# Kernel optimization log

Hardware: AMD Instinct MI355X
Metric: run time of the kernel (lower is better)

## Reference

```python
import jax, jax.numpy as jnp
import numpy as np

B, S, T = 32, 64, 48
E = 128          # embed size
H = 256          # encoder hidden (per direction)
HD = 512         # decoder hidden = 2*H
V = 32001        # vocab_size + 1


def setup_inputs() -> dict:
    key = jax.random.key(0)
    ks = jax.random.split(key, 20)
    p = lambda k, shp: jax.random.normal(k, shp, dtype=jnp.float32) * 0.05
    inp = {}
    inp["input_sequence"] = jax.random.randint(ks[0], (B, S), 0, V)
    lengths = jax.random.randint(ks[1], (B,), 1, S + 1).at[0].set(S)
    inp["input_seq_lengths"] = lengths
    inp["output_sequence"] = jax.random.randint(ks[2], (B, T), 0, V)
    # encoder params
    inp["emb_src"] = p(ks[3], (V, E))
    inp["Wih_f"] = p(ks[4], (4 * H, E)); inp["Whh_f"] = p(ks[5], (4 * H, H)); inp["b_f"] = p(ks[6], (4 * H,))
    inp["Wih_b"] = p(ks[7], (4 * H, E)); inp["Whh_b"] = p(ks[8], (4 * H, H)); inp["b_b"] = p(ks[9], (4 * H,))
    # decoder params
    inp["emb_tgt"] = p(ks[10], (V, E))
    inp["Wih_d"] = p(ks[11], (4 * HD, E)); inp["Whh_d"] = p(ks[12], (4 * HD, HD)); inp["b_d"] = p(ks[13], (4 * HD,))
    inp["W1"] = p(ks[14], (HD, HD)); inp["W2"] = p(ks[15], (HD, HD)); inp["v"] = p(ks[16], (HD,))
    inp["Wo"] = p(ks[17], (V, HD)); inp["bo"] = p(ks[18], (V,))
    return inp


def _cell(x, h, c, Wih, Whh, b):
    # PyTorch LSTM gate order: i, f, g, o. b = b_ih + b_hh.
    g = x @ Wih.T + h @ Whh.T + b
    i, f, gg, o = jnp.split(g, 4, axis=-1)
    c = jax.nn.sigmoid(f) * c + jax.nn.sigmoid(i) * jnp.tanh(gg)
    h = jax.nn.sigmoid(o) * jnp.tanh(c)
    return h, c


def reference(input_sequence, input_seq_lengths, output_sequence,
              emb_src, Wih_f, Whh_f, b_f, Wih_b, Whh_b, b_b,
              emb_tgt, Wih_d, Whh_d, b_d, W1, W2, v, Wo, bo):
    x = emb_src[input_sequence]                       # [B,S,E]
    valid = jnp.arange(S)[None, :] < input_seq_lengths[:, None]  # [B,S]
    xs = jnp.swapaxes(x, 0, 1)                        # [S,B,E]
    vs = valid.T                                      # [S,B]
    z = jnp.zeros((B, H), jnp.float32)

    def fstep(carry, inp):
        h, c = carry
        xt, vt = inp
        h, c = _cell(xt, h, c, Wih_f, Whh_f, b_f)
        return (h, c), jnp.where(vt[:, None], h, 0.0)

    _, of = jax.lax.scan(fstep, (z, z), (xs, vs))

    def bstep(carry, inp):
        # backward direction of a packed LSTM: state starts at each sequence's
        # last valid token (state held at zero while t >= length)
        h, c = carry
        xt, vt = inp
        hn, cn = _cell(xt, h, c, Wih_b, Whh_b, b_b)
        m = vt[:, None]
        h = jnp.where(m, hn, h)
        c = jnp.where(m, cn, c)
        return (h, c), jnp.where(m, h, 0.0)

    _, ob = jax.lax.scan(bstep, (z, z), (xs[::-1], vs[::-1]))
    ob = ob[::-1]
    enc = jnp.swapaxes(jnp.concatenate([of, ob], axis=-1), 0, 1)  # [B,S,512], zeros at pads

    key_proj = enc @ W1.T                             # precompute W1(key): [B,S,512]

    tgt_emb = emb_tgt[output_sequence]                # [B,T,E]
    dec_in = jnp.concatenate([jnp.zeros((B, 1, E), jnp.float32), tgt_emb[:, :-1]], axis=1)
    dec_xs = jnp.swapaxes(dec_in, 0, 1)               # [T,B,E]

    def dstep(carry, xt):
        h, c = carry
        h, c = _cell(xt, h, c, Wih_d, Whh_d, b_d)
        qp = h @ W2.T                                 # [B,512]
        energy = jnp.tanh(key_proj + qp[:, None, :]) @ v   # [B,S]
        energy = jnp.where(valid, energy, -1e10)
        w = jax.nn.softmax(energy, axis=1)
        ctx = jnp.einsum('bs,bsd->bd', w, enc)        # [B,512]
        logits = (h + ctx) @ Wo.T + bo                # [B,V]
        return (h, c), logits

    z2 = jnp.zeros((B, HD), jnp.float32)
    _, logits = jax.lax.scan(dstep, (z2, z2), dec_xs)
    outputs = jnp.swapaxes(logits, 0, 1)              # [B,T,V]

    # CrossEntropyLoss(ignore_index=0), mean over non-ignored targets
    logp = jax.nn.log_softmax(outputs, axis=-1)
    nll = -jnp.take_along_axis(logp, output_sequence[:, :, None], axis=-1)[..., 0]
    m = (output_sequence != 0).astype(jnp.float32)
    loss = jnp.sum(nll * m) / jnp.maximum(jnp.sum(m), 1.0)
    return outputs, loss
```

## Files before the change

### kernel.cpp

```cpp
#include <hip/hip_runtime.h>


typedef unsigned short ushort_t;
typedef unsigned int   uint_t;
typedef __attribute__((ext_vector_type(8))) short bf16x8;
typedef __attribute__((ext_vector_type(4))) float f32x4;

#define DEV static __device__ __forceinline__

#define NB 32
#define NS 64
#define NT 48
#define NE 128
#define NH 256
#define ND 512
#define NV 32001

#define OFF_GF   0ull
#define OFF_GB   8388608ull
#define OFF_GD   16777216ull
#define OFF_KP   29360128ull
#define OFF_CWO  0ull
#define OFF_QP   33554432ull
#define OFF_ENC  36700160ull
#define OFF_HBF  38797312ull
#define OFF_ACTX 40370176ull
#define OFF_XEE  41943040ull
#define OFF_XED  42467328ull
#define OFF_CWF  42860544ull
#define OFF_CWB  43122688ull
#define OFF_CWD  43384832ull
#define OFF_CW1  43909120ull
#define OFF_CW2  44433408ull
#define OFF_HBE  44957696ull
#define OFF_HBD  45023232ull
#define OFF_MISC 45088768ull

DEV float b2f(ushort_t u) { return __uint_as_float(((uint_t)u) << 16); }
DEV ushort_t f2b(float f) {
  uint_t x = __float_as_uint(f);
  return (ushort_t)((x + 0x7fffu + ((x >> 16) & 1u)) >> 16);
}
DEV float fsig(float x) { return 1.f / (1.f + __expf(-x)); }
DEV float ftanh(float x) { float e = __expf(2.f * x); return 1.f - 2.f / (e + 1.f); }

DEV f32x4 mfma16(bf16x8 a, bf16x8 b, f32x4 c) {
  return __builtin_amdgcn_mfma_f32_16x16x32_bf16(a, b, c, 0, 0, 0);
}
DEV void async16(void* lds, const void* g) {
  __builtin_amdgcn_global_load_lds(
      (const __attribute__((address_space(1))) uint_t*)g,
      (__attribute__((address_space(3))) uint_t*)lds, 16, 0, 0);
}
DEV bf16x8 ldw8(const float* p) {
  f32x4 a = *(const f32x4*)p;
  f32x4 b = *(const f32x4*)(p + 4);
  bf16x8 r;
  r[0] = (short)f2b(a[0]); r[1] = (short)f2b(a[1]);
  r[2] = (short)f2b(a[2]); r[3] = (short)f2b(a[3]);
  r[4] = (short)f2b(b[0]); r[5] = (short)f2b(b[1]);
  r[6] = (short)f2b(b[2]); r[7] = (short)f2b(b[3]);
  return r;
}

__global__ void init_ws(uint_t* misc) {
  for (int i = threadIdx.x; i < 1024; i += 256) misc[i] = 0u;
}

__global__ __launch_bounds__(256) void cvt_bf16(const float* __restrict__ src,
                                                ushort_t* __restrict__ dst,
                                                int n4) {
  int i = blockIdx.x * 256 + threadIdx.x;
  if (i < n4) {
    f32x4 x = *(const f32x4*)(src + (size_t)i * 4);
    uint_t lo = ((uint_t)f2b(x[1]) << 16) | (uint_t)f2b(x[0]);
    uint_t hi = ((uint_t)f2b(x[3]) << 16) | (uint_t)f2b(x[2]);
    uint2 v; v.x = lo; v.y = hi;
    *(uint2*)(dst + (size_t)i * 4) = v;
  }
}

__global__ __launch_bounds__(128) void gather_enc(const float* __restrict__ emb,
                                                  const int* __restrict__ seq,
                                                  ushort_t* __restrict__ xe) {
  int m = blockIdx.x;
  int s = m >> 5, b = m & 31;
  int tok = seq[b * NS + s];
  xe[(size_t)m * NE + threadIdx.x] = f2b(emb[(size_t)tok * NE + threadIdx.x]);
}
__global__ __launch_bounds__(128) void gather_dec(const float* __restrict__ emb,
                                                  const int* __restrict__ seq,
                                                  ushort_t* __restrict__ xe) {
  int m = blockIdx.x;
  int t = m >> 5, b = m & 31;
  float v = 0.f;
  if (t > 0) v = emb[(size_t)seq[b * NT + t - 1] * NE + threadIdx.x];
  xe[(size_t)m * NE + threadIdx.x] = f2b(v);
}

template <int CMODE, int BIAS>
__global__ __launch_bounds__(256, 2) void gemm_nt(
    const ushort_t* __restrict__ Abase, const ushort_t* __restrict__ Bmat,
    const float* __restrict__ bias, float* __restrict__ Cf,
    int N, int K, int Nvalid) {
  const int tid = threadIdx.x;
  const int wv = tid >> 6, l = tid & 63, c15 = l & 15, q = l >> 4;
  const int mw = wv >> 1, nw = wv & 1;
  const int n0 = blockIdx.x * 128, m0 = blockIdx.y * 128;
  __shared__ __align__(16) ushort_t lds[32 * 512];

  f32x4 acc[4][4];
  const f32x4 zz = {0.f, 0.f, 0.f, 0.f};
#pragma unroll
  for (int i = 0; i < 4; ++i)
#pragma unroll
    for (int j = 0; j < 4; ++j) acc[i][j] = zz;

  for (int k0 = 0; k0 < K; k0 += 64) {
    __syncthreads();
#pragma unroll
    for (int i = 0; i < 4; ++i) {
      const int slot = wv * 4 + i;
      const int kt = slot >> 3, mt = slot & 7;
      const int m = m0 + mt * 16 + c15;
      async16(&lds[slot * 512], Abase + (size_t)m * K + k0 + kt * 32 + q * 8);
      int n = n0 + mt * 16 + c15;
      if (n >= Nvalid) n = Nvalid - 1;
      async16(&lds[(16 + slot) * 512], Bmat + (size_t)n * K + k0 + kt * 32 + q * 8);
    }
    __syncthreads();
#pragma unroll
    for (int kt = 0; kt < 2; ++kt) {
      bf16x8 af[4], bfr[4];
#pragma unroll
      for (int i = 0; i < 4; ++i)
        af[i] = *(const bf16x8*)&lds[(kt * 8 + mw * 4 + i) * 512 + l * 8];
#pragma unroll
      for (int i = 0; i < 4; ++i)
        bfr[i] = *(const bf16x8*)&lds[(16 + kt * 8 + nw * 4 + i) * 512 + l * 8];
#pragma unroll
      for (int mi = 0; mi < 4; ++mi)
#pragma unroll
        for (int ni = 0; ni < 4; ++ni)
          acc[mi][ni] = mfma16(af[mi], bfr[ni], acc[mi][ni]);
    }
  }
#pragma unroll
  for (int mi = 0; mi < 4; ++mi)
#pragma unroll
    for (int ni = 0; ni < 4; ++ni) {
      const int n = n0 + (nw * 4 + ni) * 16 + c15;
      float bv = 0.f;
      if (BIAS) { if (CMODE != 2 || n < Nvalid) bv = bias[n]; }
#pragma unroll
      for (int r = 0; r < 4; ++r) {
        const int m = m0 + (mw * 4 + mi) * 16 + q * 4 + r;
        const float val = acc[mi][ni][r] + bv;
        if (CMODE == 0) Cf[(size_t)m * N + n] = val;
        else if (CMODE == 1) Cf[((size_t)(m >> 5) * N + n) * 32 + (m & 31)] = val;
        else if (n < Nvalid) Cf[(size_t)m * (size_t)NV + n] = val;
      }
    }
}

__global__ __launch_bounds__(512, 2) void enc_scan(
    const float* __restrict__ WhhF, const float* __restrict__ WhhB,
    const float* __restrict__ gF, const float* __restrict__ gB,
    const int* __restrict__ lens, ushort_t* __restrict__ enc_bf,
    ushort_t* __restrict__ hbuf, int* __restrict__ flags) {
  const int tid = threadIdx.x;
  const int d = blockIdx.x >> 1, p = blockIdx.x & 1;
  const int w = tid >> 6, l = tid & 63, c = l & 15, q = l >> 4;
  const float* Whh = d ? WhhB : WhhF;
  const float* gpre = d ? gB : gF;
  ushort_t* hb_base = hbuf + (size_t)d * 2 * 8192;
  int* flag = flags + d;
  const int u = p * 128 + w * 16 + c;

  bf16x8 wf[4][8];
#pragma unroll
  for (int g = 0; g < 4; ++g)
#pragma unroll
    for (int kt = 0; kt < 8; ++kt)
      wf[g][kt] = ldw8(Whh + (size_t)(g * 256 + u) * 256 + kt * 32 + q * 8);

  __shared__ __align__(16) ushort_t hsh[8192];
  for (int i = tid; i < 8192; i += 512) hsh[i] = 0;
  float cst[8], hst[8];
#pragma unroll
  for (int i = 0; i < 8; ++i) { cst[i] = 0.f; hst[i] = 0.f; }
  int lensr[8];
#pragma unroll
  for (int mt = 0; mt < 2; ++mt)
#pragma unroll
    for (int r = 0; r < 4; ++r) lensr[mt * 4 + r] = lens[mt * 16 + q * 4 + r];
  const int kt_u = u >> 5, j_u = u & 7, hi16 = ((u >> 3) & 3) << 4;
  __syncthreads();

  int tgt = 0;
#pragma unroll 1
  for (int s = 0; s < 64; ++s) {
    const int so = d ? (63 - s) : s;
    f32x4 acc[4][2];
#pragma unroll
    for (int g = 0; g < 4; ++g) {
      const float* gp = gpre + ((size_t)so * 1024 + (g * 256 + u)) * 32 + q * 4;
      acc[g][0] = *(const f32x4*)gp;
      acc[g][1] = *(const f32x4*)(gp + 16);
    }
#pragma unroll
    for (int kt = 0; kt < 8; ++kt) {
      bf16x8 a0 = *(const bf16x8*)&hsh[kt * 512 + l * 8];
      bf16x8 a1 = *(const bf16x8*)&hsh[(8 + kt) * 512 + l * 8];
#pragma unroll
      for (int g = 0; g < 4; ++g) {
        acc[g][0] = mfma16(a0, wf[g][kt], acc[g][0]);
        acc[g][1] = mfma16(a1, wf[g][kt], acc[g][1]);
      }
    }
    ushort_t* hbw = hb_base + (s & 1) * 8192;
#pragma unroll
    for (int mt = 0; mt < 2; ++mt)
#pragma unroll
      for (int r = 0; r < 4; ++r) {
        const int k8 = mt * 4 + r;
        const int bi = mt * 16 + q * 4 + r;
        float gi = acc[0][mt][r], gf = acc[1][mt][r];
        float gg = acc[2][mt][r], go = acc[3][mt][r];
        float ctn = fsig(gf) * cst[k8] + fsig(gi) * ftanh(gg);
        float hn = fsig(go) * ftanh(ctn);
        bool valid = so < lensr[k8];
        bool upd = (d == 0) || valid;
        cst[k8] = upd ? ctn : cst[k8];
        hst[k8] = upd ? hn : hst[k8];
        enc_bf[((size_t)bi * 64 + so) * 512 + d * 256 + u] = f2b(valid ? hn : 0.f);
        hbw[((mt * 8 + kt_u) * 64 + ((bi & 15) | hi16)) * 8 + j_u] = f2b(hst[k8]);
      }
    __syncthreads();
    if (tid == 0)
      __hip_atomic_fetch_add(flag, 1, __ATOMIC_RELEASE, __HIP_MEMORY_SCOPE_AGENT);
    tgt += 2;
    if (tid == 0) {
      while (__hip_atomic_load(flag, __ATOMIC_ACQUIRE, __HIP_MEMORY_SCOPE_AGENT) < tgt)
        __builtin_amdgcn_s_sleep(1);
    }
    __syncthreads();
    (void)__hip_atomic_load(flag, __ATOMIC_ACQUIRE, __HIP_MEMORY_SCOPE_AGENT);
    for (int i = tid; i < 1024; i += 512)
      ((uint4*)hsh)[i] = ((const uint4*)hbw)[i];
    __syncthreads();
  }
}

__global__ __launch_bounds__(512, 2) void dec_scan(
    const float* __restrict__ Whh, const float* __restrict__ gpre,
    ushort_t* __restrict__ h_bf, ushort_t* __restrict__ hbuf,
    int* __restrict__ flag) {
  const int tid = threadIdx.x;
  const int bb = blockIdx.x;
  const int w = tid >> 6, l = tid & 63, c = l & 15, q = l >> 4;
  const int uu = bb * 64 + w * 8 + (c & 7);
  const int row0 = ((c >> 3)) * 512 + uu;
  const int row1 = (2 + (c >> 3)) * 512 + uu;

  bf16x8 wf0[16], wf1[16];
#pragma unroll
  for (int kt = 0; kt < 16; ++kt) {
    wf0[kt] = ldw8(Whh + (size_t)row0 * 512 + kt * 32 + q * 8);
    wf1[kt] = ldw8(Whh + (size_t)row1 * 512 + kt * 32 + q * 8);
  }
  __shared__ __align__(16) ushort_t hsh[16384];
  for (int i = tid; i < 16384; i += 512) hsh[i] = 0;
  float cst[8];
#pragma unroll
  for (int i = 0; i < 8; ++i) cst[i] = 0.f;
  const int kt_u = uu >> 5, j_u = uu & 7, hi16 = ((uu >> 3) & 3) << 4;
  __syncthreads();

  int tgt = 0;
#pragma unroll 1
  for (int t = 0; t < 48; ++t) {
    f32x4 acc[2][2];
    {
      const float* gp0 = gpre + ((size_t)t * 2048 + row0) * 32 + q * 4;
      const float* gp1 = gpre + ((size_t)t * 2048 + row1) * 32 + q * 4;
      acc[0][0] = *(const f32x4*)gp0; acc[0][1] = *(const f32x4*)(gp0 + 16);
      acc[1][0] = *(const f32x4*)gp1; acc[1][1] = *(const f32x4*)(gp1 + 16);
    }
#pragma unroll
    for (int kt = 0; kt < 16; ++kt) {
      bf16x8 a0 = *(const bf16x8*)&hsh[kt * 512 + l * 8];
      bf16x8 a1 = *(const bf16x8*)&hsh[(16 + kt) * 512 + l * 8];
      acc[0][0] = mfma16(a0, wf0[kt], acc[0][0]);
      acc[0][1] = mfma16(a1, wf0[kt], acc[0][1]);
      acc[1][0] = mfma16(a0, wf1[kt], acc[1][0]);
      acc[1][1] = mfma16(a1, wf1[kt], acc[1][1]);
    }
    ushort_t* hbw = hbuf + (t & 1) * 16384;
#pragma unroll
    for (int mt = 0; mt < 2; ++mt)
#pragma unroll
      for (int r = 0; r < 4; ++r) {
        const int k8 = mt * 4 + r;
        const int bi = mt * 16 + q * 4 + r;
        float x0 = acc[0][mt][r];
        float x1 = acc[1][mt][r];
        float Av = fsig(x0) * ftanh(x1);
        float Ar = __shfl_xor(Av, 8, 64);
        if (c >= 8) {
          float ctn = fsig(x0) * cst[k8] + Ar;
          float hn = fsig(x1) * ftanh(ctn);
          cst[k8] = ctn;
          ushort_t hb16 = f2b(hn);
          h_bf[((size_t)t * 32 + bi) * 512 + uu] = hb16;
          hbw[((mt * 16 + kt_u) * 64 + ((bi & 15) | hi16)) * 8 + j_u] = hb16;
        }
      }
    __syncthreads();
    if (tid == 0)
      __hip_atomic_fetch_add(flag, 1, __ATOMIC_RELEASE, __HIP_MEMORY_SCOPE_AGENT);
    tgt += 8;
    if (tid == 0) {
      while (__hip_atomic_load(flag, __ATOMIC_ACQUIRE, __HIP_MEMORY_SCOPE_AGENT) < tgt)
        __builtin_amdgcn_s_sleep(1);
    }
    __syncthreads();
    (void)__hip_atomic_load(flag, __ATOMIC_ACQUIRE, __HIP_MEMORY_SCOPE_AGENT);
    for (int i = tid; i < 2048; i += 512)
      ((uint4*)hsh)[i] = ((const uint4*)hbw)[i];
    __syncthreads();
  }
}

__global__ __launch_bounds__(256) void attn_k(
    const float* __restrict__ qp, const float* __restrict__ kp,
    const ushort_t* __restrict__ enc_bf, const ushort_t* __restrict__ h_bf,
    const float* __restrict__ vvec, const int* __restrict__ lens,
    ushort_t* __restrict__ actx) {
  const int bid = blockIdx.x;
  const int b = bid / NT, t = bid % NT;
  const int tid = threadIdx.x;
  __shared__ float qps[512], vs[512], es[64];
  {
    const float* qrow = qp + ((size_t)t * 32 + b) * 512;
    float2 x = *(const float2*)&qrow[tid * 2];
    qps[tid * 2] = x.x; qps[tid * 2 + 1] = x.y;
    float2 vv = *(const float2*)&vvec[tid * 2];
    vs[tid * 2] = vv.x; vs[tid * 2 + 1] = vv.y;
  }
  __syncthreads();
  const int s = tid >> 2, i = tid & 3;
  const int len = lens[b];
  {
    const float* kr = kp + ((size_t)b * 64 + s) * 512 + i * 128;
    float e = 0.f;
#pragma unroll 8
    for (int k = 0; k < 128; k += 4) {
      f32x4 x = *(const f32x4*)&kr[k];
      const int ko = i * 128 + k;
      e += ftanh(x[0] + qps[ko]) * vs[ko];
      e += ftanh(x[1] + qps[ko + 1]) * vs[ko + 1];
      e += ftanh(x[2] + qps[ko + 2]) * vs[ko + 2];
      e += ftanh(x[3] + qps[ko + 3]) * vs[ko + 3];
    }
    e += __shfl_xor(e, 1, 64);
    e += __shfl_xor(e, 2, 64);
    if (i == 0) es[s] = (s < len) ? e : -1e10f;
  }
  __syncthreads();
  if (tid < 64) {
    float x = es[tid], m = x;
#pragma unroll
    for (int o = 1; o < 64; o <<= 1) m = fmaxf(m, __shfl_xor(m, o, 64));
    float pe = __expf(x - m), sum = pe;
#pragma unroll
    for (int o = 1; o < 64; o <<= 1) sum += __shfl_xor(sum, o, 64);
    es[tid] = pe / sum;
  }
  __syncthreads();
  const int d0 = tid * 2;
  float a0 = 0.f, a1 = 0.f;
  const ushort_t* erow = enc_bf + (size_t)b * 64 * 512 + d0;
#pragma unroll 4
  for (int ss = 0; ss < 64; ++ss) {
    uint_t uv = *(const uint_t*)(erow + (size_t)ss * 512);
    float wgt = es[ss];
    a0 += wgt * b2f((ushort_t)(uv & 0xffff));
    a1 += wgt * b2f((ushort_t)(uv >> 16));
  }
  uint_t hu = *(const uint_t*)(h_bf + ((size_t)t * 32 + b) * 512 + d0);
  float o0 = a0 + b2f((ushort_t)(hu & 0xffff));
  float o1 = a1 + b2f((ushort_t)(hu >> 16));
  uint_t packed = ((uint_t)f2b(o1) << 16) | (uint_t)f2b(o0);
  *(uint_t*)(actx + ((size_t)b * NT + t) * 512 + d0) = packed;
}

__global__ __launch_bounds__(256) void loss_k(const float* __restrict__ outp,
                                              const int* __restrict__ oseq,
                                              float* __restrict__ acc) {
  const int m = blockIdx.x;
  const int b = m / NT, t = m % NT;
  const int tid = threadIdx.x;
  const float* row = outp + (size_t)m * NV;
  __shared__ float redA[4], redB[4];
  float mx = -1e30f;
  for (int v = tid; v < NV; v += 256) mx = fmaxf(mx, row[v]);
#pragma unroll
  for (int o = 32; o; o >>= 1) mx = fmaxf(mx, __shfl_xor(mx, o, 64));
  if ((tid & 63) == 0) redA[tid >> 6] = mx;
  __syncthreads();
  mx = fmaxf(fmaxf(redA[0], redA[1]), fmaxf(redA[2], redA[3]));
  float sm = 0.f;
  for (int v = tid; v < NV; v += 256) sm += __expf(row[v] - mx);
#pragma unroll
  for (int o = 32; o; o >>= 1) sm += __shfl_xor(sm, o, 64);
  if ((tid & 63) == 0) redB[tid >> 6] = sm;
  __syncthreads();
  if (tid == 0) {
    float tot = redB[0] + redB[1] + redB[2] + redB[3];
    float lse = __logf(tot) + mx;
    int tok = oseq[b * NT + t];
    float nll = lse - row[tok];
    if (tok != 0) { atomicAdd(&acc[0], nll); atomicAdd(&acc[1], 1.f); }
  }
}

__global__ void finalize_loss(const float* __restrict__ acc,
                              float* __restrict__ outp) {
  if (threadIdx.x == 0)
    outp[(size_t)NB * NT * NV] = acc[0] / fmaxf(acc[1], 1.f);
}

extern "C" void kernel_launch(void* const* d_in, const int* in_sizes, int n_in,
                              void* d_out, int out_size, void* d_ws,
                              size_t ws_size, hipStream_t stream) {
  (void)in_sizes; (void)n_in; (void)out_size; (void)ws_size;
  const int* in_seq  = (const int*)d_in[0];
  const int* lens    = (const int*)d_in[1];
  const int* out_seq = (const int*)d_in[2];
  const float* emb_src = (const float*)d_in[3];
  const float* Wih_f = (const float*)d_in[4];
  const float* Whh_f = (const float*)d_in[5];
  const float* b_f   = (const float*)d_in[6];
  const float* Wih_b = (const float*)d_in[7];
  const float* Whh_b = (const float*)d_in[8];
  const float* b_b   = (const float*)d_in[9];
  const float* emb_tgt = (const float*)d_in[10];
  const float* Wih_d = (const float*)d_in[11];
  const float* Whh_d = (const float*)d_in[12];
  const float* b_d   = (const float*)d_in[13];
  const float* W1 = (const float*)d_in[14];
  const float* W2 = (const float*)d_in[15];
  const float* vv = (const float*)d_in[16];
  const float* Wo = (const float*)d_in[17];
  const float* bo = (const float*)d_in[18];

  char* ws = (char*)d_ws;
  float* g_fT    = (float*)(ws + OFF_GF);
  float* g_bT    = (float*)(ws + OFF_GB);
  float* g_dT    = (float*)(ws + OFF_GD);
  float* keyp    = (float*)(ws + OFF_KP);
  float* qp      = (float*)(ws + OFF_QP);
  ushort_t* encb = (ushort_t*)(ws + OFF_ENC);
  ushort_t* hbf  = (ushort_t*)(ws + OFF_HBF);
  ushort_t* actx = (ushort_t*)(ws + OFF_ACTX);
  ushort_t* xee  = (ushort_t*)(ws + OFF_XEE);
  ushort_t* xed  = (ushort_t*)(ws + OFF_XED);
  ushort_t* c_wf = (ushort_t*)(ws + OFF_CWF);
  ushort_t* c_wb = (ushort_t*)(ws + OFF_CWB);
  ushort_t* c_wd = (ushort_t*)(ws + OFF_CWD);
  ushort_t* c_w1 = (ushort_t*)(ws + OFF_CW1);
  ushort_t* c_w2 = (ushort_t*)(ws + OFF_CW2);
  ushort_t* c_wo = (ushort_t*)(ws + OFF_CWO);
  ushort_t* hbe  = (ushort_t*)(ws + OFF_HBE);
  ushort_t* hbd  = (ushort_t*)(ws + OFF_HBD);
  int* flags     = (int*)(ws + OFF_MISC);
  float* accp    = (float*)(ws + OFF_MISC + 32);
  float* outp    = (float*)d_out;

  init_ws<<<1, 256, 0, stream>>>((uint_t*)(ws + OFF_MISC));
  gather_enc<<<NB * NS, 128, 0, stream>>>(emb_src, in_seq, xee);
  gather_dec<<<NB * NT, 128, 0, stream>>>(emb_tgt, out_seq, xed);
  cvt_bf16<<<128, 256, 0, stream>>>(Wih_f, c_wf, 32768);
  cvt_bf16<<<128, 256, 0, stream>>>(Wih_b, c_wb, 32768);
  cvt_bf16<<<256, 256, 0, stream>>>(Wih_d, c_wd, 65536);
  cvt_bf16<<<256, 256, 0, stream>>>(W1, c_w1, 65536);
  cvt_bf16<<<256, 256, 0, stream>>>(W2, c_w2, 65536);
  gemm_nt<1, 1><<<dim3(8, 16), 256, 0, stream>>>(
      xee, c_wf, b_f, g_fT, 1024, 128, 1024);
  gemm_nt<1, 1><<<dim3(8, 16), 256, 0, stream>>>(
      xee, c_wb, b_b, g_bT, 1024, 128, 1024);
  gemm_nt<1, 1><<<dim3(16, 12), 256, 0, stream>>>(
      xed, c_wd, b_d, g_dT, 2048, 128, 2048);
  enc_scan<<<4, 512, 0, stream>>>(Whh_f, Whh_b, g_fT, g_bT, lens, encb, hbe, flags);
  gemm_nt<0, 0><<<dim3(4, 16), 256, 0, stream>>>(
      encb, c_w1, nullptr, keyp, 512, 512, 512);
  dec_scan<<<8, 512, 0, stream>>>(Whh_d, g_dT, hbf, hbd, flags + 2);
  gemm_nt<0, 0><<<dim3(4, 12), 256, 0, stream>>>(
      hbf, c_w2, nullptr, qp, 512, 512, 512);
  attn_k<<<NB * NT, 256, 0, stream>>>(qp, keyp, encb, hbf, vv, lens, actx);
  cvt_bf16<<<16001, 256, 0, stream>>>(Wo, c_wo, 4096128);
  gemm_nt<2, 1><<<dim3(251, 12), 256, 0, stream>>>(
      actx, c_wo, bo, outp, NV, 512, NV);
  loss_k<<<NB * NT, 256, 0, stream>>>(outp, out_seq, accp);
  finalize_loss<<<1, 64, 0, stream>>>(accp, outp);
}
```

Measured before the change: 1.465 ms.

## Single-block encoder scan, double-buffered LDS, prefetched gates, online-softmax loss

The encoder scan now runs one 1024-thread block per direction, so the hidden state stays in double-buffered LDS and the global flag-based inter-block barrier is gone. The decoder scan prefetches the next step's gate preactivations and double-buffers its LDS. It now publishes only its own hidden slice, using relaxed agent-scope 8-byte atomics and a vmcnt wait in place of acquire/release ordering. The loss kernel merges the max and sum-exp passes into one online-softmax pass that reads the logits once. In exchange, the relaxed-ordering handshake is riskier to get right, and 1024-thread blocks with large register-resident weights may limit occupancy or spill.

After: 2.250 ms. 53.6% more time.

```diff
diff --git a/kernel.cpp b/kernel.cpp
--- a/kernel.cpp
+++ b/kernel.cpp
@@ -3,6 +3,7 @@
 
 typedef unsigned short ushort_t;
 typedef unsigned int   uint_t;
+typedef unsigned long long ull_t;
 typedef __attribute__((ext_vector_type(8))) short bf16x8;
 typedef __attribute__((ext_vector_type(4))) float f32x4;
 
@@ -63,6 +64,13 @@
   return r;
 }
 
+DEV void st8_cc(void* p, ull_t v) {
+  __hip_atomic_store((ull_t*)p, v, __ATOMIC_RELAXED, __HIP_MEMORY_SCOPE_AGENT);
+}
+DEV ull_t ld8_cc(const void* p) {
+  return __hip_atomic_load((ull_t*)p, __ATOMIC_RELAXED, __HIP_MEMORY_SCOPE_AGENT);
+}
+
 __global__ void init_ws(uint_t* misc) {
   for (int i = threadIdx.x; i < 1024; i += 256) misc[i] = 0u;
 }
@@ -163,19 +171,16 @@
     }
 }
 
-__global__ __launch_bounds__(512, 2) void enc_scan(
+__global__ __launch_bounds__(1024, 1) void enc_scan(
     const float* __restrict__ WhhF, const float* __restrict__ WhhB,
     const float* __restrict__ gF, const float* __restrict__ gB,
-    const int* __restrict__ lens, ushort_t* __restrict__ enc_bf,
-    ushort_t* __restrict__ hbuf, int* __restrict__ flags) {
+    const int* __restrict__ lens, ushort_t* __restrict__ enc_bf) {
   const int tid = threadIdx.x;
-  const int d = blockIdx.x >> 1, p = blockIdx.x & 1;
+  const int d = blockIdx.x;
   const int w = tid >> 6, l = tid & 63, c = l & 15, q = l >> 4;
   const float* Whh = d ? WhhB : WhhF;
   const float* gpre = d ? gB : gF;
-  ushort_t* hb_base = hbuf + (size_t)d * 2 * 8192;
-  int* flag = flags + d;
-  const int u = p * 128 + w * 16 + c;
+  const int u = w * 16 + c;
 
   bf16x8 wf[4][8];
 #pragma unroll
@@ -184,8 +189,8 @@
     for (int kt = 0; kt < 8; ++kt)
       wf[g][kt] = ldw8(Whh + (size_t)(g * 256 + u) * 256 + kt * 32 + q * 8);
 
-  __shared__ __align__(16) ushort_t hsh[8192];
-  for (int i = tid; i < 8192; i += 512) hsh[i] = 0;
+  __shared__ __align__(16) ushort_t hsh[2][8192];
+  for (int i = tid; i < 8192; i += 1024) hsh[0][i] = 0;
   float cst[8], hst[8];
 #pragma unroll
   for (int i = 0; i < 8; ++i) { cst[i] = 0.f; hst[i] = 0.f; }
@@ -195,30 +200,45 @@
 #pragma unroll
     for (int r = 0; r < 4; ++r) lensr[mt * 4 + r] = lens[mt * 16 + q * 4 + r];
   const int kt_u = u >> 5, j_u = u & 7, hi16 = ((u >> 3) & 3) << 4;
+
+  f32x4 gv[4][2];
+  {
+    const int so0 = d ? 63 : 0;
+#pragma unroll
+    for (int g = 0; g < 4; ++g) {
+      const float* gp = gpre + ((size_t)so0 * 1024 + (g * 256 + u)) * 32 + q * 4;
+      gv[g][0] = *(const f32x4*)gp;
+      gv[g][1] = *(const f32x4*)(gp + 16);
+    }
+  }
   __syncthreads();
 
-  int tgt = 0;
 #pragma unroll 1
   for (int s = 0; s < 64; ++s) {
     const int so = d ? (63 - s) : s;
+    const int rb = s & 1;
     f32x4 acc[4][2];
 #pragma unroll
-    for (int g = 0; g < 4; ++g) {
-      const float* gp = gpre + ((size_t)so * 1024 + (g * 256 + u)) * 32 + q * 4;
-      acc[g][0] = *(const f32x4*)gp;
-      acc[g][1] = *(const f32x4*)(gp + 16);
+    for (int g = 0; g < 4; ++g) { acc[g][0] = gv[g][0]; acc[g][1] = gv[g][1]; }
+    if (s < 63) {
+      const int son = d ? (62 - s) : (s + 1);
+#pragma unroll
+      for (int g = 0; g < 4; ++g) {
+        const float* gp = gpre + ((size_t)son * 1024 + (g * 256 + u)) * 32 + q * 4;
+        gv[g][0] = *(const f32x4*)gp;
+        gv[g][1] = *(const f32x4*)(gp + 16);
+      }
     }
 #pragma unroll
     for (int kt = 0; kt < 8; ++kt) {
-      bf16x8 a0 = *(const bf16x8*)&hsh[kt * 512 + l * 8];
-      bf16x8 a1 = *(const bf16x8*)&hsh[(8 + kt) * 512 + l * 8];
+      bf16x8 a0 = *(const bf16x8*)&hsh[rb][kt * 512 + l * 8];
+      bf16x8 a1 = *(const bf16x8*)&hsh[rb][(8 + kt) * 512 + l * 8];
 #pragma unroll
       for (int g = 0; g < 4; ++g) {
         acc[g][0] = mfma16(a0, wf[g][kt], acc[g][0]);
         acc[g][1] = mfma16(a1, wf[g][kt], acc[g][1]);
       }
     }
-    ushort_t* hbw = hb_base + (s & 1) * 8192;
 #pragma unroll
     for (int mt = 0; mt < 2; ++mt)
 #pragma unroll
@@ -234,20 +254,9 @@
         cst[k8] = upd ? ctn : cst[k8];
         hst[k8] = upd ? hn : hst[k8];
         enc_bf[((size_t)bi * 64 + so) * 512 + d * 256 + u] = f2b(valid ? hn : 0.f);
-        hbw[((mt * 8 + kt_u) * 64 + ((bi & 15) | hi16)) * 8 + j_u] = f2b(hst[k8]);
+        hsh[rb ^ 1][((mt * 8 + kt_u) * 64 + ((bi & 15) | hi16)) * 8 + j_u] =
+            f2b(hst[k8]);
       }
-    __syncthreads();
-    if (tid == 0)
-      __hip_atomic_fetch_add(flag, 1, __ATOMIC_RELEASE, __HIP_MEMORY_SCOPE_AGENT);
-    tgt += 2;
-    if (tid == 0) {
-      while (__hip_atomic_load(flag, __ATOMIC_ACQUIRE, __HIP_MEMORY_SCOPE_AGENT) < tgt)
-        __builtin_amdgcn_s_sleep(1);
-    }
-    __syncthreads();
-    (void)__hip_atomic_load(flag, __ATOMIC_ACQUIRE, __HIP_MEMORY_SCOPE_AGENT);
-    for (int i = tid; i < 1024; i += 512)
-      ((uint4*)hsh)[i] = ((const uint4*)hbw)[i];
     __syncthreads();
   }
 }
@@ -269,34 +278,44 @@
     wf0[kt] = ldw8(Whh + (size_t)row0 * 512 + kt * 32 + q * 8);
     wf1[kt] = ldw8(Whh + (size_t)row1 * 512 + kt * 32 + q * 8);
   }
-  __shared__ __align__(16) ushort_t hsh[16384];
-  for (int i = tid; i < 16384; i += 512) hsh[i] = 0;
+  __shared__ __align__(16) ushort_t hsh[2][16384];
+  for (int i = tid; i < 16384; i += 512) hsh[0][i] = 0;
   float cst[8];
 #pragma unroll
   for (int i = 0; i < 8; ++i) cst[i] = 0.f;
   const int kt_u = uu >> 5, j_u = uu & 7, hi16 = ((uu >> 3) & 3) << 4;
+
+  f32x4 ga[2], gb[2];
+  {
+    const float* p0 = gpre + (size_t)row0 * 32 + q * 4;
+    const float* p1 = gpre + (size_t)row1 * 32 + q * 4;
+    ga[0] = *(const f32x4*)p0; ga[1] = *(const f32x4*)(p0 + 16);
+    gb[0] = *(const f32x4*)p1; gb[1] = *(const f32x4*)(p1 + 16);
+  }
   __syncthreads();
 
   int tgt = 0;
 #pragma unroll 1
   for (int t = 0; t < 48; ++t) {
+    const int rb = t & 1, nb = rb ^ 1;
     f32x4 acc[2][2];
-    {
-      const float* gp0 = gpre + ((size_t)t * 2048 + row0) * 32 + q * 4;
-      const float* gp1 = gpre + ((size_t)t * 2048 + row1) * 32 + q * 4;
-      acc[0][0] = *(const f32x4*)gp0; acc[0][1] = *(const f32x4*)(gp0 + 16);
-      acc[1][0] = *(const f32x4*)gp1; acc[1][1] = *(const f32x4*)(gp1 + 16);
+    acc[0][0] = ga[0]; acc[0][1] = ga[1];
+    acc[1][0] = gb[0]; acc[1][1] = gb[1];
+    if (t < 47) {
+      const float* p0 = gpre + ((size_t)(t + 1) * 2048 + row0) * 32 + q * 4;
+      const float* p1 = gpre + ((size_t)(t + 1) * 2048 + row1) * 32 + q * 4;
+      ga[0] = *(const f32x4*)p0; ga[1] = *(const f32x4*)(p0 + 16);
+      gb[0] = *(const f32x4*)p1; gb[1] = *(const f32x4*)(p1 + 16);
     }
 #pragma unroll
     for (int kt = 0; kt < 16; ++kt) {
-      bf16x8 a0 = *(const bf16x8*)&hsh[kt * 512 + l * 8];
-      bf16x8 a1 = *(const bf16x8*)&hsh[(16 + kt) * 512 + l * 8];
+      bf16x8 a0 = *(const bf16x8*)&hsh[rb][kt * 512 + l * 8];
+      bf16x8 a1 = *(const bf16x8*)&hsh[rb][(16 + kt) * 512 + l * 8];
       acc[0][0] = mfma16(a0, wf0[kt], acc[0][0]);
       acc[0][1] = mfma16(a1, wf0[kt], acc[0][1]);
       acc[1][0] = mfma16(a0, wf1[kt], acc[1][0]);
       acc[1][1] = mfma16(a1, wf1[kt], acc[1][1]);
     }
-    ushort_t* hbw = hbuf + (t & 1) * 16384;
 #pragma unroll
     for (int mt = 0; mt < 2; ++mt)
 #pragma unroll
@@ -313,21 +332,38 @@
           cst[k8] = ctn;
           ushort_t hb16 = f2b(hn);
           h_bf[((size_t)t * 32 + bi) * 512 + uu] = hb16;
-          hbw[((mt * 16 + kt_u) * 64 + ((bi & 15) | hi16)) * 8 + j_u] = hb16;
+          hsh[nb][((mt * 16 + kt_u) * 64 + ((bi & 15) | hi16)) * 8 + j_u] = hb16;
         }
       }
-    __syncthreads();
-    if (tid == 0)
-      __hip_atomic_fetch_add(flag, 1, __ATOMIC_RELEASE, __HIP_MEMORY_SCOPE_AGENT);
+    if (t == 47) break;
+    __syncthreads();
+
+    ushort_t* hbw = hbuf + nb * 16384;
+    {
+      const int chunk = tid >> 7, word = tid & 127;
+      const int mt = chunk >> 1, ktl = chunk & 1;
+      const size_t off = ((size_t)(mt * 16 + bb * 2 + ktl) * 512) + (size_t)word * 4;
+      ull_t v = *(const ull_t*)&hsh[nb][off];
+      st8_cc(hbw + off, v);
+    }
+    asm volatile("s_waitcnt vmcnt(0)" ::: "memory");
+    __syncthreads();
     tgt += 8;
     if (tid == 0) {
-      while (__hip_atomic_load(flag, __ATOMIC_ACQUIRE, __HIP_MEMORY_SCOPE_AGENT) < tgt)
+      __hip_atomic_fetch_add(flag, 1, __ATOMIC_RELAXED, __HIP_MEMORY_SCOPE_AGENT);
+      while (__hip_atomic_load(flag, __ATOMIC_RELAXED, __HIP_MEMORY_SCOPE_AGENT) < tgt)
         __builtin_amdgcn_s_sleep(1);
     }
     __syncthreads();
-    (void)__hip_atomic_load(flag, __ATOMIC_ACQUIRE, __HIP_MEMORY_SCOPE_AGENT);
-    for (int i = tid; i < 2048; i += 512)
-      ((uint4*)hsh)[i] = ((const uint4*)hbw)[i];
+    {
+      ull_t tv[8];
+#pragma unroll
+      for (int j = 0; j < 8; ++j)
+        tv[j] = ld8_cc((const ull_t*)hbw + tid + j * 512);
+#pragma unroll
+      for (int j = 0; j < 8; ++j)
+        ((ull_t*)&hsh[nb][0])[tid + j * 512] = tv[j];
+    }
     __syncthreads();
   }
 }
@@ -402,23 +438,33 @@
   const int b = m / NT, t = m % NT;
   const int tid = threadIdx.x;
   const float* row = outp + (size_t)m * NV;
-  __shared__ float redA[4], redB[4];
-  float mx = -1e30f;
-  for (int v = tid; v < NV; v += 256) mx = fmaxf(mx, row[v]);
-#pragma unroll
-  for (int o = 32; o; o >>= 1) mx = fmaxf(mx, __shfl_xor(mx, o, 64));
-  if ((tid & 63) == 0) redA[tid >> 6] = mx;
-  __syncthreads();
-  mx = fmaxf(fmaxf(redA[0], redA[1]), fmaxf(redA[2], redA[3]));
-  float sm = 0.f;
-  for (int v = tid; v < NV; v += 256) sm += __expf(row[v] - mx);
-#pragma unroll
-  for (int o = 32; o; o >>= 1) sm += __shfl_xor(sm, o, 64);
-  if ((tid & 63) == 0) redB[tid >> 6] = sm;
+  __shared__ float redM[4], redS[4];
+  float mx = -1e30f, sm = 0.f;
+  for (int v = tid; v < NV; v += 256) {
+    float x = row[v];
+    float m2 = fmaxf(mx, x);
+    sm = sm * __expf(mx - m2) + __expf(x - m2);
+    mx = m2;
+  }
+#pragma unroll
+  for (int o = 1; o < 64; o <<= 1) {
+    float mo = __shfl_xor(mx, o, 64);
+    float so = __shfl_xor(sm, o, 64);
+    float m2 = fmaxf(mx, mo);
+    sm = sm * __expf(mx - m2) + so * __expf(mo - m2);
+    mx = m2;
+  }
+  if ((tid & 63) == 0) { redM[tid >> 6] = mx; redS[tid >> 6] = sm; }
   __syncthreads();
   if (tid == 0) {
-    float tot = redB[0] + redB[1] + redB[2] + redB[3];
-    float lse = __logf(tot) + mx;
+    float M = redM[0], S = redS[0];
+#pragma unroll
+    for (int i = 1; i < 4; ++i) {
+      float m2 = fmaxf(M, redM[i]);
+      S = S * __expf(M - m2) + redS[i] * __expf(redM[i] - m2);
+      M = m2;
+    }
+    float lse = __logf(S) + M;
     int tok = oseq[b * NT + t];
     float nll = lse - row[tok];
     if (tok != 0) { atomicAdd(&acc[0], nll); atomicAdd(&acc[1], 1.f); }
@@ -472,7 +518,6 @@
   ushort_t* c_w1 = (ushort_t*)(ws + OFF_CW1);
   ushort_t* c_w2 = (ushort_t*)(ws + OFF_CW2);
   ushort_t* c_wo = (ushort_t*)(ws + OFF_CWO);
-  ushort_t* hbe  = (ushort_t*)(ws + OFF_HBE);
   ushort_t* hbd  = (ushort_t*)(ws + OFF_HBD);
   int* flags     = (int*)(ws + OFF_MISC);
   float* accp    = (float*)(ws + OFF_MISC + 32);
@@ -492,7 +537,7 @@
       xee, c_wb, b_b, g_bT, 1024, 128, 1024);
   gemm_nt<1, 1><<<dim3(16, 12), 256, 0, stream>>>(
       xed, c_wd, b_d, g_dT, 2048, 128, 2048);
-  enc_scan<<<4, 512, 0, stream>>>(Whh_f, Whh_b, g_fT, g_bT, lens, encb, hbe, flags);
+  enc_scan<<<2, 1024, 0, stream>>>(Whh_f, Whh_b, g_fT, g_bT, lens, encb);
   gemm_nt<0, 0><<<dim3(4, 16), 256, 0, stream>>>(
       encb, c_w1, nullptr, keyp, 512, 512, 512);
   dec_scan<<<8, 512, 0, stream>>>(Whh_d, g_dT, hbf, hbd, flags + 2);
```
